# Kernel optimization log

Hardware: AMD Instinct MI355X
Metric: run time of the kernel (lower is better)

Reference implementation:

```python
import jax, jax.numpy as jnp
import numpy as np

N_NODES = 16384
N_FEAT = 16384
EMBED = 64
BATCH = 4096
N_EDGES = 524288


def setup_inputs() -> dict:
    key = jax.random.key(0)
    k1, k2, k3, k4, k5 = jax.random.split(key, 5)
    x = jax.random.randint(k1, (BATCH, 2), 0, N_NODES, dtype=jnp.int64)
    X = jax.random.normal(k2, (N_NODES, N_FEAT), dtype=jnp.float32) * 0.05
    edge_index = jax.random.randint(k3, (2, N_EDGES), 0, N_NODES, dtype=jnp.int64)
    W_gcn = jax.random.normal(k4, (N_FEAT, EMBED), dtype=jnp.float32) * (1.0 / np.sqrt(N_FEAT))
    b_gcn = jnp.zeros((EMBED,), dtype=jnp.float32)
    w_lin = jax.random.normal(k5, (N_NODES, 1), dtype=jnp.float32) * 0.01
    b_lin = jnp.zeros((1,), dtype=jnp.float32)
    return {"x": x, "X": X, "edge_index": edge_index, "W_gcn": W_gcn,
            "b_gcn": b_gcn, "w_lin": w_lin, "b_lin": b_lin}


def _gcn_conv(X, edge_index, W, b):
    """PyG GCNConv: symmetric-normalized aggregation with self-loops."""
    n = X.shape[0]
    xw = X @ W  # [N, D] -- dominant GEMM
    loop = jnp.arange(n)
    src = jnp.concatenate([edge_index[0], loop])
    dst = jnp.concatenate([edge_index[1], loop])
    deg = jax.ops.segment_sum(jnp.ones_like(dst, dtype=xw.dtype), dst, num_segments=n)
    dinv = jnp.where(deg > 0, jax.lax.rsqrt(deg), 0.0)
    norm = dinv[src] * dinv[dst]  # [E+N]
    out = jax.ops.segment_sum(xw[src] * norm[:, None], dst, num_segments=n)
    return out + b


def reference(x, X, edge_index, W_gcn, b_gcn, w_lin, b_lin):
    emb_all = _gcn_conv(X, edge_index, W_gcn, b_gcn)  # [N, D]
    emb = emb_all[x]  # [B, 2, D]
    # FM pairwise interaction: 0.5 * sum((sum_i v)^2 - sum_i v^2)
    sq_of_sum = jnp.sum(emb, axis=1) ** 2       # [B, D]
    sum_of_sq = jnp.sum(emb ** 2, axis=1)       # [B, D]
    fm = 0.5 * jnp.sum(sq_of_sum - sum_of_sq, axis=1, keepdims=True)  # [B, 1]
    lin = jnp.sum(w_lin[x], axis=1) + b_lin      # [B, 1]
    return (lin + fm).squeeze(1)                 # [B]
```

## Files before the change

### kernel.cpp

```cpp
#include <hip/hip_runtime.h>
#include <cstddef>

#define N_NODES 16384
#define N_FEAT  16384
#define EMBED   64
#define BATCH   4096
#define N_EDGES 524288

typedef __attribute__((ext_vector_type(8))) short bf16x8;
typedef __attribute__((ext_vector_type(4))) float f32x4;

__device__ __forceinline__ ushort f32_to_bf16(float f) {
    unsigned u = __float_as_uint(f);
    return (ushort)((u + 0x7FFFu + ((u >> 16) & 1u)) >> 16);
}
__device__ __forceinline__ float bf16_to_f32(ushort h) {
    return __uint_as_float((unsigned)h << 16);
}

__global__ void k_deg_init(float* __restrict__ deg) {
    int n = blockIdx.x * blockDim.x + threadIdx.x;
    if (n < N_NODES) deg[n] = 1.0f;
}
__global__ void k_deg_acc(const int* __restrict__ ei, float* __restrict__ deg) {
    int e = blockIdx.x * blockDim.x + threadIdx.x;
    if (e < N_EDGES) atomicAdd(&deg[ei[N_EDGES + e]], 1.0f);
}
__global__ void k_dinv(float* __restrict__ deg) {
    int n = blockIdx.x * blockDim.x + threadIdx.x;
    if (n < N_NODES) deg[n] = rsqrtf(deg[n]);
}

__global__ __launch_bounds__(1024) void k_scan(const float* __restrict__ deg,
                                               int* __restrict__ off,
                                               int* __restrict__ cur) {
    __shared__ int part[1024];
    const int t = threadIdx.x;
    int c[16];
    int s = 0;
    #pragma unroll
    for (int i = 0; i < 16; ++i) {
        c[i] = (int)deg[t * 16 + i] - 1;
        s += c[i];
    }
    part[t] = s;
    __syncthreads();
    for (int d = 1; d < 1024; d <<= 1) {
        int v = (t >= d) ? part[t - d] : 0;
        __syncthreads();
        part[t] += v;
        __syncthreads();
    }
    int run = (t == 0) ? 0 : part[t - 1];
    #pragma unroll
    for (int i = 0; i < 16; ++i) {
        off[t * 16 + i] = run;
        cur[t * 16 + i] = run;
        run += c[i];
    }
    if (t == 1023) off[N_NODES] = run;
}

__global__ void k_scatter(const int* __restrict__ ei, int* __restrict__ cur,
                          int* __restrict__ srcs) {
    int e = blockIdx.x * blockDim.x + threadIdx.x;
    if (e < N_EDGES) {
        int s = ei[e];
        int d = ei[N_EDGES + e];
        srcs[atomicAdd(&cur[d], 1)] = s;
    }
}

__global__ void k_wpack(const float* __restrict__ W, short* __restrict__ Wpk) {
    int tid = blockIdx.x * blockDim.x + threadIdx.x;
    int lane = tid & 63;
    int f = tid >> 6;
    int ct = f & 3;
    int ks = (f >> 2) & 511;
    int sp = f >> 11;
    int n = ct * 16 + (lane & 15);
    int kbase = ks * 32 + (lane >> 4) * 8;
    bf16x8 r;
    #pragma unroll
    for (int j = 0; j < 8; ++j) {
        float w = W[(size_t)(kbase + j) * EMBED + n];
        ushort h = f32_to_bf16(w);
        r[j] = (sp == 0) ? (short)h : (short)f32_to_bf16(w - bf16_to_f32(h));
    }
    *(bf16x8*)(Wpk + (size_t)f * 512 + lane * 8) = r;
}

__global__ void k_zero(float4* __restrict__ p) {
    p[blockIdx.x * blockDim.x + threadIdx.x] = make_float4(0.f, 0.f, 0.f, 0.f);
}

#define GBM 128
#define KSPLIT 4
#define KCHUNK (N_FEAT / KSPLIT)

__global__ __launch_bounds__(256, 2) void k_gemm(const float* __restrict__ X,
                                                 const short* __restrict__ Wpk,
                                                 float* __restrict__ xw) {
    __shared__ ushort Xh[GBM][40];
    __shared__ ushort Xl[GBM][40];

    const int t = threadIdx.x;
    const int rb = blockIdx.x & 127;
    const int ks0 = (blockIdx.x >> 7) * (KCHUNK / 32);
    const int block_row = rb * GBM;
    const int w = t >> 6;
    const int lane = t & 63;
    const int g = lane >> 4;
    const int lr = lane & 15;
    const int srow = t >> 3;
    const int sq = t & 7;

    f32x4 acc[2][4] = {};

    for (int kt = 0; kt < KCHUNK / 32; ++kt) {
        const int kstep = ks0 + kt;
        const int k0 = kstep * 32;

        bf16x8 bh[4], bl[4];
        #pragma unroll
        for (int ct = 0; ct < 4; ++ct) {
            const short* p = Wpk + (size_t)(kstep * 4 + ct) * 512 + lane * 8;
            bh[ct] = *(const bf16x8*)p;
            bl[ct] = *(const bf16x8*)(p + 1048576);
        }

        float4 v[4];
        #pragma unroll
        for (int i = 0; i < 4; ++i)
            v[i] = *(const float4*)(X + (size_t)(block_row + srow + i * 32) * N_FEAT + k0 + sq * 4);

        #pragma unroll
        for (int i = 0; i < 4; ++i) {
            float vv[4] = {v[i].x, v[i].y, v[i].z, v[i].w};
            ushort4 hv, lv;
            ushort* hp = (ushort*)&hv;
            ushort* lp = (ushort*)&lv;
            #pragma unroll
            for (int e = 0; e < 4; ++e) {
                ushort h = f32_to_bf16(vv[e]);
                hp[e] = h;
                lp[e] = f32_to_bf16(vv[e] - bf16_to_f32(h));
            }
            int row = srow + i * 32;
            *(ushort4*)(&Xh[row][sq * 4]) = hv;
            *(ushort4*)(&Xl[row][sq * 4]) = lv;
        }
        __syncthreads();

        bf16x8 ah[2], al[2];
        #pragma unroll
        for (int rt = 0; rt < 2; ++rt) {
            int row = w * 32 + rt * 16 + lr;
            ah[rt] = *(const bf16x8*)(&Xh[row][g * 8]);
            al[rt] = *(const bf16x8*)(&Xl[row][g * 8]);
        }
        #pragma unroll
        for (int rt = 0; rt < 2; ++rt) {
            #pragma unroll
            for (int ct = 0; ct < 4; ++ct) {
                acc[rt][ct] = __builtin_amdgcn_mfma_f32_16x16x32_bf16(ah[rt], bh[ct], acc[rt][ct], 0, 0, 0);
                acc[rt][ct] = __builtin_amdgcn_mfma_f32_16x16x32_bf16(ah[rt], bl[ct], acc[rt][ct], 0, 0, 0);
                acc[rt][ct] = __builtin_amdgcn_mfma_f32_16x16x32_bf16(al[rt], bh[ct], acc[rt][ct], 0, 0, 0);
            }
        }
        __syncthreads();
    }

    #pragma unroll
    for (int rt = 0; rt < 2; ++rt)
        #pragma unroll
        for (int ct = 0; ct < 4; ++ct)
            #pragma unroll
            for (int r = 0; r < 4; ++r) {
                int row = block_row + w * 32 + rt * 16 + g * 4 + r;
                atomicAdd(&xw[(size_t)row * EMBED + ct * 16 + lr], acc[rt][ct][r]);
            }
}

__global__ void k_gather(const int* __restrict__ off, const int* __restrict__ srcs,
                         const float* __restrict__ xw, const float* __restrict__ dinv,
                         float* __restrict__ agg) {
    int n = blockIdx.x * 4 + (threadIdx.x >> 6);
    int lane = threadIdx.x & 63;
    float dn = dinv[n];
    float acc = xw[(size_t)n * EMBED + lane] * dn;
    int i = off[n], i1 = off[n + 1];
    for (; i + 1 < i1; i += 2) {
        int s0 = srcs[i], s1 = srcs[i + 1];
        float a0 = xw[(size_t)s0 * EMBED + lane] * dinv[s0];
        float a1 = xw[(size_t)s1 * EMBED + lane] * dinv[s1];
        acc += a0 + a1;
    }
    if (i < i1) {
        int s = srcs[i];
        acc += xw[(size_t)s * EMBED + lane] * dinv[s];
    }
    agg[(size_t)n * EMBED + lane] = acc * dn;
}

__global__ void k_final(const int* __restrict__ x, const float* __restrict__ agg,
                        const float* __restrict__ b_gcn, const float* __restrict__ w_lin,
                        const float* __restrict__ b_lin, float* __restrict__ out) {
    int b = blockIdx.x * (blockDim.x >> 6) + (threadIdx.x >> 6);
    int lane = threadIdx.x & 63;
    if (b >= BATCH) return;
    int i0 = x[2 * b + 0];
    int i1 = x[2 * b + 1];
    float bg = b_gcn[lane];
    float e0 = agg[(size_t)i0 * EMBED + lane] + bg;
    float e1 = agg[(size_t)i1 * EMBED + lane] + bg;
    float p = e0 * e1;
    #pragma unroll
    for (int off = 32; off > 0; off >>= 1) p += __shfl_down(p, off, 64);
    if (lane == 0) out[b] = p + w_lin[i0] + w_lin[i1] + b_lin[0];
}

extern "C" void kernel_launch(void* const* d_in, const int* in_sizes, int n_in,
                              void* d_out, int out_size, void* d_ws, size_t ws_size,
                              hipStream_t stream) {
    (void)in_sizes; (void)n_in; (void)out_size; (void)ws_size;

    const int*   x   = (const int*)d_in[0];
    const float* X   = (const float*)d_in[1];
    const int*   ei  = (const int*)d_in[2];
    const float* W   = (const float*)d_in[3];
    const float* bg  = (const float*)d_in[4];
    const float* wl  = (const float*)d_in[5];
    const float* bl  = (const float*)d_in[6];
    float* out = (float*)d_out;

    char* ws = (char*)d_ws;
    float* xw   = (float*)(ws);
    float* agg  = (float*)(ws + (size_t)(4 << 20));
    short* Wpk  = (short*)(ws + (size_t)(4 << 20));
    float* dinv = (float*)(ws + (size_t)(8 << 20));
    int*   off  = (int*)  (ws + (size_t)(8 << 20) + (1 << 17));
    int*   cur  = (int*)  (ws + (size_t)(8 << 20) + (1 << 18));
    int*   srcs = (int*)  (ws + (size_t)(8 << 20) + (1 << 19));

    k_deg_init<<<N_NODES / 256, 256, 0, stream>>>(dinv);
    k_deg_acc<<<N_EDGES / 256, 256, 0, stream>>>(ei, dinv);
    k_scan<<<1, 1024, 0, stream>>>(dinv, off, cur);
    k_dinv<<<N_NODES / 256, 256, 0, stream>>>(dinv);
    k_scatter<<<N_EDGES / 256, 256, 0, stream>>>(ei, cur, srcs);

    k_wpack<<<1024, 256, 0, stream>>>(W, Wpk);
    k_zero<<<1024, 256, 0, stream>>>((float4*)xw);
    k_gemm<<<(N_NODES / GBM) * KSPLIT, 256, 0, stream>>>(X, Wpk, xw);

    k_gather<<<N_NODES / 4, 256, 0, stream>>>(off, srcs, xw, dinv, agg);
    k_final<<<BATCH / 4, 256, 0, stream>>>(x, agg, bg, wl, bl, out);
}
```

Baseline: 1.504 ms.

## Double-buffer X tiles via direct global-to-LDS loads and split-K partial buffers

The GEMM now stages raw fp32 X tiles straight into swizzled LDS through global_load_lds, with double buffering so the next tile loads while the current one is computed. The bf16 hi/lo split moves to after the LDS read. KSPLIT rises to 8 and occupancy to 4 blocks per SM. Atomic accumulation is replaced by per-split partial buffers plus a separate reduce kernel, which adds 32MB of partial traffic and one more launch but removes the atomics and the zero-fill kernel.

Measured after the change: 1.501 ms. Within noise of the previous version (-0.2%).

```diff
diff --git a/kernel.cpp b/kernel.cpp
--- a/kernel.cpp
+++ b/kernel.cpp
@@ -16,6 +16,16 @@
 }
 __device__ __forceinline__ float bf16_to_f32(ushort h) {
     return __uint_as_float((unsigned)h << 16);
+}
+
+__device__ __forceinline__ void split8(float4 a, float4 b, bf16x8& h, bf16x8& l) {
+    float f[8] = {a.x, a.y, a.z, a.w, b.x, b.y, b.z, b.w};
+    #pragma unroll
+    for (int j = 0; j < 8; ++j) {
+        ushort hh = f32_to_bf16(f[j]);
+        h[j] = (short)hh;
+        l[j] = (short)f32_to_bf16(f[j] - bf16_to_f32(hh));
+    }
 }
 
 __global__ void k_deg_init(float* __restrict__ deg) {
@@ -90,75 +100,71 @@
     *(bf16x8*)(Wpk + (size_t)f * 512 + lane * 8) = r;
 }
 
-__global__ void k_zero(float4* __restrict__ p) {
-    p[blockIdx.x * blockDim.x + threadIdx.x] = make_float4(0.f, 0.f, 0.f, 0.f);
-}
-
 #define GBM 128
-#define KSPLIT 4
+#define KSPLIT 8
 #define KCHUNK (N_FEAT / KSPLIT)
-
-__global__ __launch_bounds__(256, 2) void k_gemm(const float* __restrict__ X,
+#define NSTEP (KCHUNK / 32)
+
+__global__ __launch_bounds__(256, 4) void k_gemm(const float* __restrict__ X,
                                                  const short* __restrict__ Wpk,
-                                                 float* __restrict__ xw) {
-    __shared__ ushort Xh[GBM][40];
-    __shared__ ushort Xl[GBM][40];
+                                                 float* __restrict__ xw_part) {
+    __shared__ float Xs[2][GBM][32];
 
     const int t = threadIdx.x;
-    const int rb = blockIdx.x & 127;
-    const int ks0 = (blockIdx.x >> 7) * (KCHUNK / 32);
+    const int kpl = blockIdx.x & 7;
+    const int rb = blockIdx.x >> 3;
     const int block_row = rb * GBM;
     const int w = t >> 6;
     const int lane = t & 63;
     const int g = lane >> 4;
     const int lr = lane & 15;
-    const int srow = t >> 3;
-    const int sq = t & 7;
+    const int swz = lr & 7;
+
+    const int rsub = lane >> 3;
+    const int qsrc = (lane & 7) ^ rsub;
+    const float* gl = X + (size_t)(block_row + w * 32 + rsub) * N_FEAT
+                        + (size_t)kpl * KCHUNK + qsrc * 4;
 
     f32x4 acc[2][4] = {};
-
-    for (int kt = 0; kt < KCHUNK / 32; ++kt) {
-        const int kstep = ks0 + kt;
-        const int k0 = kstep * 32;
-
+    int cur = 0;
+
+#define STAGE(buf, kt)                                                          \
+    {                                                                           \
+        _Pragma("unroll")                                                       \
+        for (int i = 0; i < 4; ++i)                                             \
+            __builtin_amdgcn_global_load_lds(                                   \
+                (const __attribute__((address_space(1))) void*)                 \
+                    (gl + (size_t)i * 8 * N_FEAT + (kt) * 32),                  \
+                (__attribute__((address_space(3))) void*)&Xs[buf][w * 32 + i * 8][0], \
+                16, 0, 0);                                                      \
+    }
+
+    STAGE(0, 0);
+    __syncthreads();
+
+    for (int kt = 0; kt < NSTEP; ++kt) {
+        if (kt + 1 < NSTEP) STAGE(cur ^ 1, kt + 1);
+
+        const int kstep = kpl * NSTEP + kt;
+        const short* bp = Wpk + (size_t)(kstep * 4) * 512 + lane * 8;
         bf16x8 bh[4], bl[4];
         #pragma unroll
         for (int ct = 0; ct < 4; ++ct) {
-            const short* p = Wpk + (size_t)(kstep * 4 + ct) * 512 + lane * 8;
-            bh[ct] = *(const bf16x8*)p;
-            bl[ct] = *(const bf16x8*)(p + 1048576);
+            bh[ct] = *(const bf16x8*)(bp + ct * 512);
+            bl[ct] = *(const bf16x8*)(bp + ct * 512 + 1048576);
         }
 
-        float4 v[4];
-        #pragma unroll
-        for (int i = 0; i < 4; ++i)
-            v[i] = *(const float4*)(X + (size_t)(block_row + srow + i * 32) * N_FEAT + k0 + sq * 4);
-
-        #pragma unroll
-        for (int i = 0; i < 4; ++i) {
-            float vv[4] = {v[i].x, v[i].y, v[i].z, v[i].w};
-            ushort4 hv, lv;
-            ushort* hp = (ushort*)&hv;
-            ushort* lp = (ushort*)&lv;
-            #pragma unroll
-            for (int e = 0; e < 4; ++e) {
-                ushort h = f32_to_bf16(vv[e]);
-                hp[e] = h;
-                lp[e] = f32_to_bf16(vv[e] - bf16_to_f32(h));
-            }
-            int row = srow + i * 32;
-            *(ushort4*)(&Xh[row][sq * 4]) = hv;
-            *(ushort4*)(&Xl[row][sq * 4]) = lv;
-        }
-        __syncthreads();
-
+        const int q0 = ((2 * g) ^ swz) * 4;
+        const int q1 = ((2 * g + 1) ^ swz) * 4;
+        const int r0 = w * 32 + lr;
+        float4 x0 = *(const float4*)&Xs[cur][r0][q0];
+        float4 x1 = *(const float4*)&Xs[cur][r0][q1];
+        float4 x2 = *(const float4*)&Xs[cur][r0 + 16][q0];
+        float4 x3 = *(const float4*)&Xs[cur][r0 + 16][q1];
         bf16x8 ah[2], al[2];
-        #pragma unroll
-        for (int rt = 0; rt < 2; ++rt) {
-            int row = w * 32 + rt * 16 + lr;
-            ah[rt] = *(const bf16x8*)(&Xh[row][g * 8]);
-            al[rt] = *(const bf16x8*)(&Xl[row][g * 8]);
-        }
+        split8(x0, x1, ah[0], al[0]);
+        split8(x2, x3, ah[1], al[1]);
+
         #pragma unroll
         for (int rt = 0; rt < 2; ++rt) {
             #pragma unroll
@@ -169,8 +175,11 @@
             }
         }
         __syncthreads();
-    }
-
+        cur ^= 1;
+    }
+#undef STAGE
+
+    float* part = xw_part + (size_t)kpl * (N_NODES * EMBED);
     #pragma unroll
     for (int rt = 0; rt < 2; ++rt)
         #pragma unroll
@@ -178,8 +187,19 @@
             #pragma unroll
             for (int r = 0; r < 4; ++r) {
                 int row = block_row + w * 32 + rt * 16 + g * 4 + r;
-                atomicAdd(&xw[(size_t)row * EMBED + ct * 16 + lr], acc[rt][ct][r]);
+                part[(size_t)row * EMBED + ct * 16 + lr] = acc[rt][ct][r];
             }
+}
+
+__global__ void k_reduce(const float4* __restrict__ part, float4* __restrict__ xw) {
+    int i = blockIdx.x * blockDim.x + threadIdx.x;
+    float4 s = part[i];
+    #pragma unroll
+    for (int p = 1; p < KSPLIT; ++p) {
+        float4 v = part[(size_t)p * (N_NODES * EMBED / 4) + i];
+        s.x += v.x; s.y += v.y; s.z += v.z; s.w += v.w;
+    }
+    xw[i] = s;
 }
 
 __global__ void k_gather(const int* __restrict__ off, const int* __restrict__ srcs,
@@ -235,13 +255,14 @@
     float* out = (float*)d_out;
 
     char* ws = (char*)d_ws;
-    float* xw   = (float*)(ws);
-    float* agg  = (float*)(ws + (size_t)(4 << 20));
-    short* Wpk  = (short*)(ws + (size_t)(4 << 20));
-    float* dinv = (float*)(ws + (size_t)(8 << 20));
-    int*   off  = (int*)  (ws + (size_t)(8 << 20) + (1 << 17));
-    int*   cur  = (int*)  (ws + (size_t)(8 << 20) + (1 << 18));
-    int*   srcs = (int*)  (ws + (size_t)(8 << 20) + (1 << 19));
+    float* xw      = (float*)(ws);
+    short* Wpk     = (short*)(ws + (size_t)(4 << 20));
+    float* agg     = (float*)(ws + (size_t)(4 << 20));
+    float* dinv    = (float*)(ws + (size_t)(8 << 20));
+    int*   off     = (int*)  (ws + (size_t)(8 << 20) + (1 << 17));
+    int*   cur     = (int*)  (ws + (size_t)(8 << 20) + (1 << 18));
+    int*   srcs    = (int*)  (ws + (size_t)(8 << 20) + (1 << 19));
+    float* xw_part = (float*)(ws + (size_t)(16 << 20));
 
     k_deg_init<<<N_NODES / 256, 256, 0, stream>>>(dinv);
     k_deg_acc<<<N_EDGES / 256, 256, 0, stream>>>(ei, dinv);
@@ -250,8 +271,8 @@
     k_scatter<<<N_EDGES / 256, 256, 0, stream>>>(ei, cur, srcs);
 
     k_wpack<<<1024, 256, 0, stream>>>(W, Wpk);
-    k_zero<<<1024, 256, 0, stream>>>((float4*)xw);
-    k_gemm<<<(N_NODES / GBM) * KSPLIT, 256, 0, stream>>>(X, Wpk, xw);
+    k_gemm<<<(N_NODES / GBM) * KSPLIT, 256, 0, stream>>>(X, Wpk, xw_part);
+    k_reduce<<<(N_NODES * EMBED / 4) / 256, 256, 0, stream>>>((const float4*)xw_part, (float4*)xw);
 
     k_gather<<<N_NODES / 4, 256, 0, stream>>>(off, srcs, xw, dinv, agg);
     k_final<<<BATCH / 4, 256, 0, stream>>>(x, agg, bg, wl, bl, out);
```
